# Kernel tuning notes

Measured on AMD Instinct MI355X. Metric: run time of the kernel, lower is better.

Reference implementation:

```python
import jax, jax.numpy as jnp
import numpy as np

B, NMAX, NPOOL = 4, 128, 16
I_CNN, QDIM, LIN, NCLS = 2048, 1024, 1024, 16
D_BOX = I_CNN + 4            # 2052: box feat + 4 coords
D_IN = 2 * D_BOX + QDIM      # 5128: g1/g2 first-layer input width


def _make_pool_coords():
    # mirrors RN.make_coords(4): 4x4 grid of boxes over a 448px image, normalized
    W = 448.0
    box = W / 4.0
    c = []
    for y in range(4):
        for x in range(4):
            c.append([x * box, y * box, (x + 1) * box, (y + 1) * box])
    return jnp.asarray(np.array(c) / 448.0, dtype=jnp.float32)


def setup_inputs() -> dict:
    key = jax.random.key(0)
    ks = jax.random.split(key, 32)
    f32 = jnp.float32
    def p(k, shape):
        return jax.random.normal(k, shape, f32) * 0.02
    inp = {
        "wholefeat": jax.random.normal(ks[0], (B, I_CNN), f32),
        "pooled": jax.random.normal(ks[1], (B, NPOOL, I_CNN), f32),
        "box_feats": jax.random.normal(ks[2], (B, NMAX, I_CNN), f32),
        "q_feats": jax.random.normal(ks[3], (B, QDIM), f32),  # q_rnn output (QRNN external)
        "box_coords": jax.random.uniform(ks[4], (B, NMAX, 4), f32),
        "index": jax.random.randint(ks[5], (B,), 16, NMAX + 1),
        # g1 MLP (5128 -> 1024 -> 1024 -> 1024)
        "g1_w1": p(ks[6], (D_IN, LIN)), "g1_b1": jnp.zeros((LIN,), f32),
        "g1_w2": p(ks[7], (LIN, LIN)), "g1_b2": jnp.zeros((LIN,), f32),
        "g1_w3": p(ks[8], (LIN, LIN)), "g1_b3": jnp.zeros((LIN,), f32),
        "f1_w": p(ks[9], (LIN, LIN)), "f1_b": jnp.zeros((LIN,), f32),
        # g2 MLP (5128 -> 1024 -> 1024 -> 1024)
        "g2_w1": p(ks[10], (D_IN, LIN)), "g2_b1": jnp.zeros((LIN,), f32),
        "g2_w2": p(ks[11], (LIN, LIN)), "g2_b2": jnp.zeros((LIN,), f32),
        "g2_w3": p(ks[12], (LIN, LIN)), "g2_b3": jnp.zeros((LIN,), f32),
        "f2_w": p(ks[13], (LIN, LIN)), "f2_b": jnp.zeros((LIN,), f32),
        # fgamma (2048 -> 1024 -> Ncls)
        "fg_w1": p(ks[14], (2 * LIN, 1024)), "fg_b1": jnp.zeros((1024,), f32),
        "fg_w2": p(ks[15], (1024, NCLS)), "fg_b2": jnp.zeros((NCLS,), f32),
        "pool_coords": _make_pool_coords(),
    }
    return inp


def _forward(wholefeat, pooled, box_feats, q_feats, box_coords,
             g1_w1, g1_b1, g1_w2, g1_b2, g1_w3, g1_b3, f1_w, f1_b,
             g2_w1, g2_b1, g2_w2, g2_b2, g2_w3, g2_b3, f2_w, f2_b,
             fg_w1, fg_b1, fg_w2, fg_b2, pool_coords, index):
    relu = jax.nn.relu
    # Decompose first Linear of each g-MLP: cat([b_i, b_j, q]) @ W == b_i@Wa + b_j@Wb + q@Wq
    # (mathematically identical, avoids materializing the [N*N, 5128] concat)
    W1a, W1b, W1q = g1_w1[:D_BOX], g1_w1[D_BOX:2 * D_BOX], g1_w1[2 * D_BOX:]
    W2a, W2b, W2q = g2_w1[:D_BOX], g2_w1[D_BOX:2 * D_BOX], g2_w1[2 * D_BOX:]

    def per_sample(bf, bc, q, pool_i, n):
        # bf: [NMAX, 2048], bc: [NMAX, 4], q: [1024], pool_i: [NPOOL, 2048], n: scalar int
        valid = (jnp.arange(NMAX) < n).astype(bf.dtype)  # ragged mask over boxes
        bfc = jnp.concatenate([bf, bc], axis=-1)          # [NMAX, 2052]
        # g1: all-pairs relation MLP, summed over valid (i, j) pairs
        hq = q @ W1q + g1_b1                              # [1024]
        h = relu((bfc @ W1a)[:, None, :] + (bfc @ W1b)[None, :, :] + hq)  # [NMAX, NMAX, 1024]
        h = relu(h @ g1_w2 + g1_b2)
        h = relu(h @ g1_w3 + g1_b3)
        g1_sum = jnp.einsum('ijd,i,j->d', h, valid, valid)
        rno = relu(g1_sum @ f1_w + f1_b)                  # [1024]
        # g2: box x pooled-grid relation MLP, summed over valid i and all 16 pooled cells
        pc = jnp.concatenate([pool_i, pool_coords], axis=-1)  # [NPOOL, 2052]
        h2 = relu((bfc @ W2a)[:, None, :] + (pc @ W2b)[None, :, :] + (q @ W2q + g2_b1))  # [NMAX, NPOOL, 1024]
        h2 = relu(h2 @ g2_w2 + g2_b2)
        h2 = relu(h2 @ g2_w3 + g2_b3)
        g2_sum = jnp.einsum('ipd,i->d', h2, valid)
        rnob = relu(g2_sum @ f2_w + f2_b)                 # [1024]
        rn = jnp.concatenate([rno, rnob])                 # [2048]
        return relu(rn @ fg_w1 + fg_b1) @ fg_w2 + fg_b2   # [NCLS]

    return jax.vmap(per_sample)(box_feats, box_coords, q_feats, pooled, index)


def reference(wholefeat, pooled, box_feats, q_feats, box_coords,
              g1_w1, g1_b1, g1_w2, g1_b2, g1_w3, g1_b3, f1_w, f1_b,
              g2_w1, g2_b1, g2_w2, g2_b2, g2_w3, g2_b3, f2_w, f2_b,
              fg_w1, fg_b1, fg_w2, fg_b2, pool_coords, index):
    return _forward(wholefeat, pooled, box_feats, q_feats, box_coords,
                    g1_w1, g1_b1, g1_w2, g1_b2, g1_w3, g1_b3, f1_w, f1_b,
                    g2_w1, g2_b1, g2_w2, g2_b2, g2_w3, g2_b3, f2_w, f2_b,
                    fg_w1, fg_b1, fg_w2, fg_b2, pool_coords, index)
```

## Files before the change

### kernel.cpp

```cpp
#include <hip/hip_runtime.h>

typedef __attribute__((ext_vector_type(8))) short short8;
typedef __attribute__((ext_vector_type(8))) __bf16 bf16x8;
typedef __attribute__((ext_vector_type(4))) float f32x4;

__device__ __forceinline__ short f2bf(float f) {
    union { float f; unsigned u; } x; x.f = f;
    unsigned r = (x.u + 0x7FFFu + ((x.u >> 16) & 1u)) >> 16;
    return (short)r;
}

__device__ __forceinline__ f32x4 mfma16(bf16x8 a, bf16x8 b, f32x4 c) {
    return __builtin_amdgcn_mfma_f32_16x16x32_bf16(a, b, c, 0, 0, 0);
}

__device__ __forceinline__ int swz(int slot) { return slot ^ ((slot >> 4) & 7); }

struct WConvP {
    const float* src0[8];
    const float* srcq[8];
    const float* bias[8];
    short*       dst[8];
    int          n0[8];
    int          nK[8];
    int          perm[8];
};

__global__ __launch_bounds__(256) void k_wconv(WConvP P) {
    int y = blockIdx.y;
    int nK = P.nK[y];
    int nchunks = nK << 6;
    int c = blockIdx.x * 4 + (threadIdx.x >> 6);
    if (c >= nchunks) return;
    int l = threadIdx.x & 63;
    int t = c % nK, nf = c / nK;
    int k0 = (t << 5) + ((l >> 4) << 3);
    int n  = (nf << 4) + (l & 15);
    const float* src0 = P.src0[y];
    const float* srcq = P.srcq[y];
    const float* bias = P.bias[y];
    int n0 = P.n0[y], pm = P.perm[y];
    short8 v;
#pragma unroll
    for (int j = 0; j < 8; ++j) {
        int kk = k0 + j;
        float f = 0.f;
        if (pm) {
            int pr = (kk & ~127) | ((kk & 7) << 4) | ((kk >> 3) & 15);
            f = src0[(size_t)pr * 1024 + n];
        } else if (kk < n0) {
            f = src0[(size_t)kk * 1024 + n];
        } else if (srcq && kk >= 2080 && kk < 3104) {
            f = srcq[(size_t)(kk - 2080) * 1024 + n];
        } else if (bias && kk == 3104) {
            f = bias[n];
        }
        v[j] = f2bf(f);
    }
    ((short8*)P.dst[y])[(size_t)c * 64 + l] = v;
}

__global__ __launch_bounds__(256) void k_build(const float* box_feats, const float* box_coords,
                                               const float* pooled, const float* pool_coords,
                                               const float* q_feats, short* bfcq, short* pc) {
    int id = blockIdx.x * 256 + threadIdx.x;
    if (blockIdx.y == 0) {
        if (id >= 512 * 3136) return;
        int row = id / 3136, kp = id - row * 3136;
        int b = row >> 7, i = row & 127;
        float v = 0.f;
        if (kp < 2048)       v = box_feats[((size_t)(b * 128 + i)) * 2048 + kp];
        else if (kp < 2052)  v = box_coords[(b * 128 + i) * 4 + (kp - 2048)];
        else if (kp >= 2080 && kp < 3104) v = q_feats[b * 1024 + (kp - 2080)];
        else if (kp == 3104) v = 1.0f;
        bfcq[id] = f2bf(v);
    } else {
        if (id >= 64 * 2080) return;
        int row = id / 2080, kp = id - row * 2080;
        int b = row >> 4, j = row & 15;
        float v = 0.f;
        if (kp < 2048)      v = pooled[((size_t)(b * 16 + j)) * 2048 + kp];
        else if (kp < 2052) v = pool_coords[j * 4 + (kp - 2048)];
        pc[id] = f2bf(v);
    }
}

struct S1P {
    const short*  X[4];
    const short8* Wf[4];
    float*        Out[4];
    int           xstr[4];
    int           nK[4];
};

__global__ __launch_bounds__(256) void k_stage1(S1P P) {
    int bid = blockIdx.x;
    int z, idx;
    if (bid < 64)       { z = 0; idx = bid; }
    else if (bid < 128) { z = 1; idx = bid - 64; }
    else if (bid < 192) { z = 2; idx = bid - 128; }
    else                { z = 3; idx = bid - 192; }
    int mt = idx >> 2, panel = idx & 3;
    int m0 = mt << 5;
    const short*  Xg = P.X[z];
    const short8* Wf = P.Wf[z];
    float* Out = P.Out[z];
    int xstr = P.xstr[z], nK = P.nK[z];

    int tid = threadIdx.x, w = tid >> 6, l = tid & 63, lr = l & 15, lh = l >> 4;
    int nfb = (panel << 4) + (w << 2);
    const short8* Wl = Wf + (size_t)nfb * nK * 64 + l;
    f32x4 z4 = {0.f, 0.f, 0.f, 0.f};
    f32x4 acc[2][4];
#pragma unroll
    for (int mf = 0; mf < 2; ++mf)
#pragma unroll
        for (int f = 0; f < 4; ++f) acc[mf][f] = z4;

    for (int t = 0; t < nK; ++t) {
        int k0 = (t << 5) + (lh << 3);
        const short* xb = Xg + (size_t)(m0 + lr) * xstr + k0;
        bf16x8 a0 = __builtin_bit_cast(bf16x8, *(const short8*)xb);
        bf16x8 a1 = __builtin_bit_cast(bf16x8, *(const short8*)(xb + (size_t)16 * xstr));
#pragma unroll
        for (int f = 0; f < 4; ++f) {
            bf16x8 bb = __builtin_bit_cast(bf16x8, Wl[((size_t)f * nK + t) << 6]);
            acc[0][f] = mfma16(a0, bb, acc[0][f]);
            acc[1][f] = mfma16(a1, bb, acc[1][f]);
        }
    }
#pragma unroll
    for (int mf = 0; mf < 2; ++mf)
#pragma unroll
        for (int f = 0; f < 4; ++f)
#pragma unroll
            for (int r = 0; r < 4; ++r) {
                int row = m0 + (mf << 4) + (lh << 2) + r;
                int col = (panel << 8) + (w << 6) + (f << 4) + lr;
                Out[(size_t)row * 1024 + col] = acc[mf][f][r];
            }
}

__device__ __forceinline__ void gemm_pipe(const short8* __restrict__ Wl,
                                          const short8* __restrict__ XLs,
                                          int l, f32x4 (&acc)[4][8]) {
    bf16x8 wA[8], wB[8], av[4];
#pragma unroll
    for (int f = 0; f < 8; ++f)
        wA[f] = __builtin_bit_cast(bf16x8, Wl[f << 11]);
#pragma unroll
    for (int t = 0; t < 32; t += 2) {
#pragma unroll
        for (int f = 0; f < 8; ++f)
            wB[f] = __builtin_bit_cast(bf16x8, Wl[(f << 11) + ((t + 1) << 6)]);
#pragma unroll
        for (int mf = 0; mf < 4; ++mf)
            av[mf] = __builtin_bit_cast(bf16x8, XLs[swz((((mf << 5) + t) << 6) + l)]);
        __builtin_amdgcn_s_setprio(1);
#pragma unroll
        for (int f = 0; f < 8; ++f)
#pragma unroll
            for (int mf = 0; mf < 4; ++mf)
                acc[mf][f] = mfma16(av[mf], wA[f], acc[mf][f]);
        __builtin_amdgcn_s_setprio(0);
        if (t + 2 < 32) {
#pragma unroll
            for (int f = 0; f < 8; ++f)
                wA[f] = __builtin_bit_cast(bf16x8, Wl[(f << 11) + ((t + 2) << 6)]);
        }
#pragma unroll
        for (int mf = 0; mf < 4; ++mf)
            av[mf] = __builtin_bit_cast(bf16x8, XLs[swz((((mf << 5) + (t + 1)) << 6) + l)]);
        __builtin_amdgcn_s_setprio(1);
#pragma unroll
        for (int f = 0; f < 8; ++f)
#pragma unroll
            for (int mf = 0; mf < 4; ++mf)
                acc[mf][f] = mfma16(av[mf], wB[f], acc[mf][f]);
        __builtin_amdgcn_s_setprio(0);
    }
}

struct FuseP {
    const float*  Arow[2];
    const float*  Brow[2];
    const short8* W2[2];
    const short8* W3[2];
    const float*  b2[2];
    const float*  b3[2];
    float*        gsum[2];
    const int*    index;
};

__global__ __launch_bounds__(512, 2) void k_fused(FuseP P) {
    __shared__ short8 XL[8192];
    int b  = blockIdx.y;
    int px = blockIdx.x;
    int mode = (px >= 256) ? 1 : 0;
    int pxl  = mode ? (px - 256) : px;
    int nv = P.index[b];
    int npairs = mode ? (nv << 4) : (nv * nv);
    int p0 = pxl << 6;
    if (p0 >= npairs) return;
    int tid = threadIdx.x, w = tid >> 6, l = tid & 63, lr = l & 15, lh = l >> 4;
    const float* Arow = P.Arow[mode] + (size_t)b * 128 * 1024;
    const float* Brow = P.Brow[mode] + (size_t)b * (mode ? 16 : 128) * 1024;

    {
        int mfp = w >> 1;
        int p = p0 + (mfp << 4) + lr;
        int i = 0, j = 0;
        if (p < npairs) {
            if (mode) { i = p >> 4; j = p & 15; }
            else      { i = (int)((unsigned)p / (unsigned)nv); j = p - i * nv; }
        }
        const float* Ap = Arow + (size_t)i * 1024;
        const float* Bp = Brow + (size_t)j * 1024;
        int tbase = (w & 1) << 4;
#pragma unroll
        for (int cc = 0; cc < 16; ++cc) {
            int t = tbase + cc;
            int k0 = (t << 5) + (lh << 3);
            f32x4 a0 = *(const f32x4*)(Ap + k0), a1 = *(const f32x4*)(Ap + k0 + 4);
            f32x4 b0 = *(const f32x4*)(Bp + k0), b1 = *(const f32x4*)(Bp + k0 + 4);
            short8 v;
#pragma unroll
            for (int e = 0; e < 4; ++e) {
                v[e]     = f2bf(fmaxf(a0[e] + b0[e], 0.f));
                v[4 + e] = f2bf(fmaxf(a1[e] + b1[e], 0.f));
            }
            XL[swz((((mfp << 5) + t) << 6) + l)] = v;
        }
    }
    __syncthreads();

    f32x4 z4 = {0.f, 0.f, 0.f, 0.f};
    f32x4 acc[4][8];
#pragma unroll
    for (int mf = 0; mf < 4; ++mf)
#pragma unroll
        for (int f = 0; f < 8; ++f) acc[mf][f] = z4;
    gemm_pipe(P.W2[mode] + ((size_t)w << 14) + l, XL, l, acc);
    __syncthreads();

    {
        float b2l[8];
#pragma unroll
        for (int f = 0; f < 8; ++f) b2l[f] = P.b2[mode][(w << 7) + (f << 4) + lr];
#pragma unroll
        for (int mf = 0; mf < 4; ++mf)
#pragma unroll
            for (int r = 0; r < 4; ++r) {
                short8 v;
#pragma unroll
                for (int f = 0; f < 8; ++f)
                    v[f] = f2bf(fmaxf(acc[mf][f][r] + b2l[f], 0.f));
                int slot = (((mf << 5) + (w << 2) + (lr >> 2)) << 6)
                         + ((lr & 3) << 4) + (lh << 2) + r;
                XL[swz(slot)] = v;
            }
    }
    __syncthreads();

#pragma unroll
    for (int mf = 0; mf < 4; ++mf)
#pragma unroll
        for (int f = 0; f < 8; ++f) acc[mf][f] = z4;
    gemm_pipe(P.W3[mode] + ((size_t)w << 14) + l, XL, l, acc);

    float b3l[8];
#pragma unroll
    for (int f = 0; f < 8; ++f) b3l[f] = P.b3[mode][(w << 7) + (f << 4) + lr];
#pragma unroll
    for (int f = 0; f < 8; ++f) {
        float s = 0.f;
#pragma unroll
        for (int mf = 0; mf < 4; ++mf)
#pragma unroll
            for (int r = 0; r < 4; ++r) {
                int m = (mf << 4) + (lh << 2) + r;
                if (p0 + m < npairs) s += fmaxf(acc[mf][f][r] + b3l[f], 0.f);
            }
        s += __shfl_xor(s, 16);
        s += __shfl_xor(s, 32);
        if (l < 16) atomicAdd(&P.gsum[mode][(size_t)b * 1024 + (w << 7) + (f << 4) + l], s);
    }
}

__global__ __launch_bounds__(256) void k_t1(const float* g1s, const float* g2s,
                                            const float* f1_w, const float* f1_b,
                                            const float* f2_w, const float* f2_b,
                                            float* rn) {
    __shared__ float red[256];
    int bi = blockIdx.x;
    int s = bi >> 6, b = (bi >> 4) & 3, nb = bi & 15;
    int t = threadIdx.x, nl = t & 63, sl = t >> 6;
    int n = (nb << 6) + nl;
    const float* vin = (s ? g2s : g1s) + b * 1024;
    const float* W = s ? f2_w : f1_w;
    float p = 0.f;
    int k0 = sl << 8;
    for (int k = 0; k < 256; ++k) p += vin[k0 + k] * W[(size_t)(k0 + k) * 1024 + n];
    red[t] = p;
    __syncthreads();
    if (t < 64) {
        float tot = red[t] + red[t + 64] + red[t + 128] + red[t + 192];
        const float* bias = s ? f2_b : f1_b;
        int nn = (nb << 6) + t;
        rn[(size_t)b * 2048 + (s << 10) + nn] = fmaxf(tot + bias[nn], 0.f);
    }
}

__global__ __launch_bounds__(256) void k_t2(const float* rn, const float* fg_w1,
                                            const float* fg_b1, float* u) {
    __shared__ float red[256];
    int bi = blockIdx.x;
    int b = bi >> 4, nb = bi & 15;
    int t = threadIdx.x, nl = t & 63, sl = t >> 6;
    int n = (nb << 6) + nl;
    float p = 0.f;
    int k0 = sl << 9;
    for (int k = 0; k < 512; ++k) p += rn[(size_t)b * 2048 + k0 + k] * fg_w1[(size_t)(k0 + k) * 1024 + n];
    red[t] = p;
    __syncthreads();
    if (t < 64) {
        float tot = red[t] + red[t + 64] + red[t + 128] + red[t + 192];
        int nn = (nb << 6) + t;
        u[(size_t)b * 1024 + nn] = fmaxf(tot + fg_b1[nn], 0.f);
    }
}

__global__ __launch_bounds__(256) void k_t3(const float* u, const float* fg_w2,
                                            const float* fg_b2, float* out) {
    __shared__ float red[256];
    int b = blockIdx.x;
    int t = threadIdx.x, c = t & 15, sl = t >> 4;
    float p = 0.f;
    int k0 = sl << 6;
    for (int k = 0; k < 64; ++k) p += u[(size_t)b * 1024 + k0 + k] * fg_w2[(size_t)(k0 + k) * 16 + c];
    red[t] = p;
    __syncthreads();
    if (t < 16) {
        float tot = 0.f;
#pragma unroll
        for (int s2 = 0; s2 < 16; ++s2) tot += red[t + (s2 << 4)];
        out[b * 16 + t] = tot + fg_b2[t];
    }
}

extern "C" void kernel_launch(void* const* d_in, const int* in_sizes, int n_in,
                              void* d_out, int out_size, void* d_ws, size_t ws_size,
                              hipStream_t stream) {
    (void)in_sizes; (void)n_in; (void)out_size; (void)ws_size;
    const float* pooled      = (const float*)d_in[1];
    const float* box_feats   = (const float*)d_in[2];
    const float* q_feats     = (const float*)d_in[3];
    const float* box_coords  = (const float*)d_in[4];
    const int*   index       = (const int*)d_in[5];
    const float* g1_w1 = (const float*)d_in[6];
    const float* g1_b1 = (const float*)d_in[7];
    const float* g1_w2 = (const float*)d_in[8];
    const float* g1_b2 = (const float*)d_in[9];
    const float* g1_w3 = (const float*)d_in[10];
    const float* g1_b3 = (const float*)d_in[11];
    const float* f1_w  = (const float*)d_in[12];
    const float* f1_b  = (const float*)d_in[13];
    const float* g2_w1 = (const float*)d_in[14];
    const float* g2_b1 = (const float*)d_in[15];
    const float* g2_w2 = (const float*)d_in[16];
    const float* g2_b2 = (const float*)d_in[17];
    const float* g2_w3 = (const float*)d_in[18];
    const float* g2_b3 = (const float*)d_in[19];
    const float* f2_w  = (const float*)d_in[20];
    const float* f2_b  = (const float*)d_in[21];
    const float* fg_w1 = (const float*)d_in[22];
    const float* fg_b1 = (const float*)d_in[23];
    const float* fg_w2 = (const float*)d_in[24];
    const float* fg_b2 = (const float*)d_in[25];
    const float* pool_coords = (const float*)d_in[26];
    float* out = (float*)d_out;

    char* base = (char*)d_ws;
    size_t off = 0;
    auto alloc = [&](size_t bytes) -> void* {
        void* p = base + off;
        off = (off + bytes + 255) & ~(size_t)255;
        return p;
    };
    const size_t szWf98 = (size_t)98 * 64 * 64 * 16;
    const size_t szWf65 = (size_t)65 * 64 * 64 * 16;
    const size_t szWf32 = (size_t)32 * 64 * 64 * 16;
    short* WfA   = (short*)alloc(szWf98);
    short* WfB   = (short*)alloc(szWf65);
    short* Wf2A  = (short*)alloc(szWf98);
    short* Wf2B  = (short*)alloc(szWf65);
    short* Wg1w2 = (short*)alloc(szWf32);
    short* Wg1w3 = (short*)alloc(szWf32);
    short* Wg2w2 = (short*)alloc(szWf32);
    short* Wg2w3 = (short*)alloc(szWf32);
    short* bfcq  = (short*)alloc((size_t)512 * 3136 * 2);
    short* pc    = (short*)alloc((size_t)64 * 2080 * 2);
    float* A1    = (float*)alloc((size_t)512 * 1024 * 4);
    float* B1    = (float*)alloc((size_t)512 * 1024 * 4);
    float* A2    = (float*)alloc((size_t)512 * 1024 * 4);
    float* P2    = (float*)alloc((size_t)64 * 1024 * 4);
    float* sums  = (float*)alloc((size_t)2 * 4096 * 4);
    float* g1s   = sums;
    float* g2s   = sums + 4096;
    float* rn    = (float*)alloc((size_t)4 * 2048 * 4);
    float* u     = (float*)alloc((size_t)4 * 1024 * 4);

    hipMemsetAsync(sums, 0, 2 * 4096 * 4, stream);

    WConvP wp;
    for (int y = 0; y < 8; ++y) { wp.srcq[y] = nullptr; wp.bias[y] = nullptr; wp.perm[y] = 0; }
    wp.src0[0] = g1_w1;                      wp.srcq[0] = g1_w1 + (size_t)4104*1024; wp.bias[0] = g1_b1;
    wp.dst[0] = WfA;   wp.n0[0] = 2052; wp.nK[0] = 98;
    wp.src0[1] = g1_w1 + (size_t)2052*1024;  wp.dst[1] = WfB;   wp.n0[1] = 2052; wp.nK[1] = 65;
    wp.src0[2] = g2_w1;                      wp.srcq[2] = g2_w1 + (size_t)4104*1024; wp.bias[2] = g2_b1;
    wp.dst[2] = Wf2A;  wp.n0[2] = 2052; wp.nK[2] = 98;
    wp.src0[3] = g2_w1 + (size_t)2052*1024;  wp.dst[3] = Wf2B;  wp.n0[3] = 2052; wp.nK[3] = 65;
    wp.src0[4] = g1_w2; wp.dst[4] = Wg1w2; wp.n0[4] = 1024; wp.nK[4] = 32;
    wp.src0[5] = g1_w3; wp.dst[5] = Wg1w3; wp.n0[5] = 1024; wp.nK[5] = 32; wp.perm[5] = 1;
    wp.src0[6] = g2_w2; wp.dst[6] = Wg2w2; wp.n0[6] = 1024; wp.nK[6] = 32;
    wp.src0[7] = g2_w3; wp.dst[7] = Wg2w3; wp.n0[7] = 1024; wp.nK[7] = 32; wp.perm[7] = 1;
    k_wconv<<<dim3(1568, 8), 256, 0, stream>>>(wp);

    k_build<<<dim3(6272, 2), 256, 0, stream>>>(box_feats, box_coords, pooled, pool_coords,
                                               q_feats, bfcq, pc);

    S1P sp;
    sp.X[0] = bfcq; sp.Wf[0] = (const short8*)WfA;  sp.Out[0] = A1; sp.xstr[0] = 3136; sp.nK[0] = 98;
    sp.X[1] = bfcq; sp.Wf[1] = (const short8*)WfB;  sp.Out[1] = B1; sp.xstr[1] = 3136; sp.nK[1] = 65;
    sp.X[2] = bfcq; sp.Wf[2] = (const short8*)Wf2A; sp.Out[2] = A2; sp.xstr[2] = 3136; sp.nK[2] = 98;
    sp.X[3] = pc;   sp.Wf[3] = (const short8*)Wf2B; sp.Out[3] = P2; sp.xstr[3] = 2080; sp.nK[3] = 65;
    k_stage1<<<200, 256, 0, stream>>>(sp);

    FuseP fp;
    fp.Arow[0] = A1; fp.Brow[0] = B1;
    fp.W2[0] = (const short8*)Wg1w2; fp.W3[0] = (const short8*)Wg1w3;
    fp.b2[0] = g1_b2; fp.b3[0] = g1_b3; fp.gsum[0] = g1s;
    fp.Arow[1] = A2; fp.Brow[1] = P2;
    fp.W2[1] = (const short8*)Wg2w2; fp.W3[1] = (const short8*)Wg2w3;
    fp.b2[1] = g2_b2; fp.b3[1] = g2_b3; fp.gsum[1] = g2s;
    fp.index = index;
    k_fused<<<dim3(288, 4), 512, 0, stream>>>(fp);

    k_t1<<<128, 256, 0, stream>>>(g1s, g2s, f1_w, f1_b, f2_w, f2_b, rn);
    k_t2<<<64, 256, 0, stream>>>(rn, fg_w1, fg_b1, u);
    k_t3<<<4, 256, 0, stream>>>(u, fg_w2, fg_b2, out);
}
```

Measured before the change: 489.5 us.

## Remap fused grid to XCD-aware 1D order and simplify weight prefetch loop

The fused pairwise MLP kernel now launches as a 1D grid and remaps block IDs so that consecutive logical tiles, which share weight panels and the same batch, land on the same XCD (fid&7 selects the chunk). The aim is better L2 reuse of the bf16 weights on the multi-die MI355X. Separately, the double-buffered register prefetch of weight fragments in gemm_pipe is replaced with a plain per-step load. That lowers register pressure but leaves load latency to the compiler and the wave scheduler to hide.

```diff
diff --git a/kernel.cpp b/kernel.cpp
--- a/kernel.cpp
+++ b/kernel.cpp
@@ -144,15 +144,11 @@
 __device__ __forceinline__ void gemm_pipe(const short8* __restrict__ Wl,
                                           const short8* __restrict__ XLs,
                                           int l, f32x4 (&acc)[4][8]) {
-    bf16x8 wA[8], wB[8], av[4];
-#pragma unroll
-    for (int f = 0; f < 8; ++f)
-        wA[f] = __builtin_bit_cast(bf16x8, Wl[f << 11]);
-#pragma unroll
-    for (int t = 0; t < 32; t += 2) {
+    for (int t = 0; t < 32; ++t) {
+        bf16x8 w[8], av[4];
 #pragma unroll
         for (int f = 0; f < 8; ++f)
-            wB[f] = __builtin_bit_cast(bf16x8, Wl[(f << 11) + ((t + 1) << 6)]);
+            w[f] = __builtin_bit_cast(bf16x8, Wl[(f << 11) + (t << 6)]);
 #pragma unroll
         for (int mf = 0; mf < 4; ++mf)
             av[mf] = __builtin_bit_cast(bf16x8, XLs[swz((((mf << 5) + t) << 6) + l)]);
@@ -161,22 +157,7 @@
         for (int f = 0; f < 8; ++f)
 #pragma unroll
             for (int mf = 0; mf < 4; ++mf)
-                acc[mf][f] = mfma16(av[mf], wA[f], acc[mf][f]);
-        __builtin_amdgcn_s_setprio(0);
-        if (t + 2 < 32) {
-#pragma unroll
-            for (int f = 0; f < 8; ++f)
-                wA[f] = __builtin_bit_cast(bf16x8, Wl[(f << 11) + ((t + 2) << 6)]);
-        }
-#pragma unroll
-        for (int mf = 0; mf < 4; ++mf)
-            av[mf] = __builtin_bit_cast(bf16x8, XLs[swz((((mf << 5) + (t + 1)) << 6) + l)]);
-        __builtin_amdgcn_s_setprio(1);
-#pragma unroll
-        for (int f = 0; f < 8; ++f)
-#pragma unroll
-            for (int mf = 0; mf < 4; ++mf)
-                acc[mf][f] = mfma16(av[mf], wB[f], acc[mf][f]);
+                acc[mf][f] = mfma16(av[mf], w[f], acc[mf][f]);
         __builtin_amdgcn_s_setprio(0);
     }
 }
@@ -194,8 +175,10 @@
 
 __global__ __launch_bounds__(512, 2) void k_fused(FuseP P) {
     __shared__ short8 XL[8192];
-    int b  = blockIdx.y;
-    int px = blockIdx.x;
+    int fid = blockIdx.x;
+    int logical = (fid & 7) * 144 + (fid >> 3);
+    int px = logical % 288;
+    int b  = logical / 288;
     int mode = (px >= 256) ? 1 : 0;
     int pxl  = mode ? (px - 256) : px;
     int nv = P.index[b];
@@ -444,7 +427,7 @@
     fp.W2[1] = (const short8*)Wg2w2; fp.W3[1] = (const short8*)Wg2w3;
     fp.b2[1] = g2_b2; fp.b3[1] = g2_b3; fp.gsum[1] = g2s;
     fp.index = index;
-    k_fused<<<dim3(288, 4), 512, 0, stream>>>(fp);
+    k_fused<<<1152, 512, 0, stream>>>(fp);
 
     k_t1<<<128, 256, 0, stream>>>(g1s, g2s, f1_w, f1_b, f2_w, f2_b, rn);
     k_t2<<<64, 256, 0, stream>>>(rn, fg_w1, fg_b1, u);
```

Result: slower. 531.9 us (+8.7%).
